# Performance work log

Measured on AMD Instinct MI355X. Metric: run time of the kernel, lower is better.

The kernel has to match this reference:

```python
import jax, jax.numpy as jnp
import numpy as np

B, H, W, CIN, COUT, KH, KW = 16, 64, 64, 256, 256, 3, 3


def setup_inputs() -> dict:
    key = jax.random.key(0)
    k1, k2, k3 = jax.random.split(key, 3)
    x = jax.random.normal(k1, (B, H, W, CIN), dtype=jnp.float32)
    style = jax.random.normal(k2, (B, CIN), dtype=jnp.float32)
    # glorot-ish scale for the base kernel
    kernel = jax.random.normal(k3, (KH, KW, CIN, COUT), dtype=jnp.float32) * 0.05
    return {"x": x, "style": style, "kernel": kernel}


def reference(x, style, kernel):
    b = x.shape[0]
    cout = kernel.shape[-1]
    # Modulate: per-sample weights [B, kh, kw, Cin, Cout]
    w = kernel[None] * (style[:, None, None, :, None] + 1.0)
    # Demodulate: L2 normalize over (kh, kw, Cin) per (sample, out-channel)
    w = w / jnp.sqrt(jnp.sum(jnp.square(w), axis=(1, 2, 3), keepdims=True) + 1e-8)
    # Batch-as-groups grouped conv: x -> [1, B*Cin, H, W]
    xg = jnp.transpose(x, (0, 3, 1, 2)).reshape(1, -1, x.shape[1], x.shape[2])
    # w -> [kh, kw, Cin, B*Cout]
    wg = jnp.transpose(w, (1, 2, 3, 0, 4)).reshape(w.shape[1], w.shape[2], w.shape[3], -1)
    y = jax.lax.conv_general_dilated(
        xg, wg,
        window_strides=(1, 1),
        padding='SAME',
        dimension_numbers=('NCHW', 'HWIO', 'NCHW'),
        feature_group_count=b,
    )
    # [1, B*Cout, H, W] -> [B, H, W, Cout]
    y = y.reshape(b, cout, y.shape[2], y.shape[3])
    return jnp.transpose(y, (0, 2, 3, 1))
```

## Files before the change

### kernel.cpp

```cpp
#include <hip/hip_runtime.h>


#define HH 64
#define WW 64
#define CI 256
#define CO 256
#define KTOT 2304
#define CIPITCH 40
#define XCOLS 66
#define BPITCH 100

typedef float    f32x4 __attribute__((ext_vector_type(4)));
typedef _Float16 f16x8 __attribute__((ext_vector_type(8)));
typedef __fp16   fp16x2 __attribute__((ext_vector_type(2)));

__device__ __forceinline__ unsigned pk2(float a, float b) {
    fp16x2 h = __builtin_amdgcn_cvt_pkrtz(a, b);
    return __builtin_bit_cast(unsigned, h);
}

__global__ __launch_bounds__(256) void modscale_part(
    const float* __restrict__ kern,
    const float* __restrict__ style,
    float* __restrict__ scale2)
{
    const int b = blockIdx.x / 9;
    const int t = blockIdx.x - b * 9;
    const int tid = threadIdx.x;
    __shared__ float st[CI];
    st[tid] = style[b * CI + tid] + 1.0f;
    __syncthreads();
    float acc = 0.f;
    const float* kp = kern + (size_t)t * CI * CO + tid;
    #pragma unroll 8
    for (int ci = 0; ci < CI; ++ci) {
        float m = kp[ci * CO] * st[ci];
        acc += m * m;
    }
    atomicAdd(&scale2[b * CO + tid], acc);
}

__global__ __launch_bounds__(256) void prep_wt(const float* __restrict__ kern,
                                               ushort* __restrict__ Wt) {
    __shared__ ushort tile[64][65];
    const int kt = blockIdx.x >> 2;
    const int ct = blockIdx.x & 3;
    const int k0 = kt * 64, c0 = ct * 64;
    const int tid = threadIdx.x;
    const int r = tid >> 2, q = tid & 3;

    const float* src = kern + (size_t)(k0 + r) * CO + c0 + q * 16;
    #pragma unroll
    for (int j = 0; j < 16; ++j) {
        _Float16 h = (_Float16)src[j];
        tile[q * 16 + j][r] = __builtin_bit_cast(unsigned short, h);
    }
    __syncthreads();
    ushort* dst = Wt + (size_t)(c0 + r) * KTOT + k0 + q * 16;
    #pragma unroll
    for (int j = 0; j < 16; ++j) dst[j] = tile[r][q * 16 + j];
}

__global__ __launch_bounds__(256) void gemm_conv(
    const float* __restrict__ x,
    const ushort* __restrict__ Wt,
    const float* __restrict__ style,
    const float* __restrict__ scale2,
    float* __restrict__ y)
{
    __shared__ __align__(16) ushort xs[4 * XCOLS * CIPITCH];
    __shared__ __align__(16) ushort bs[128 * BPITCH];
    __shared__ float s_style[CI];

    const int tid  = threadIdx.x;
    const int lane = tid & 63;
    const int wave = tid >> 6;

    const int mtile = blockIdx.x >> 1;
    const int n0    = (blockIdx.x & 1) * 128;
    const int p0    = mtile * 128;
    const int b     = p0 >> 12;
    const int h0    = (p0 >> 6) & 63;

    s_style[tid] = style[b * CI + tid] + 1.0f;

    const int wm = (wave & 1) * 64;
    const int wn = (wave >> 1) * 64;
    const int fr = lane & 15;
    const int fq = lane >> 4;
    const int xlane = fr * CIPITCH + fq * 8;

    f32x4 acc[4][4] = {};

    for (int c = 0; c < 8; ++c) {
        __syncthreads();

        #pragma unroll
        for (int p = 0; p < 9; ++p) {
            const int task = p * 256 + tid;
            if (task < 2112) {
                const int rowcol = task >> 3;
                const int chunk  = task & 7;
                const int row = rowcol / XCOLS;
                const int col = rowcol - row * XCOLS;
                const int rg = h0 - 1 + row;
                const int cg = col - 1;
                f32x4 v = {0.f, 0.f, 0.f, 0.f};
                if ((unsigned)rg < 64u && (unsigned)cg < 64u)
                    v = *(const f32x4*)(x + ((size_t)((b * HH + rg) * WW + cg)) * CI
                                          + c * 32 + chunk * 4);
                const f32x4 st = *(const f32x4*)(s_style + c * 32 + chunk * 4);
                const f32x4 m = v * st;
                uint2 u;
                u.x = pk2(m.x, m.y);
                u.y = pk2(m.z, m.w);
                *(uint2*)(xs + rowcol * CIPITCH + chunk * 4) = u;
            }
        }

        #pragma unroll
        for (int tr = 0; tr < 3; ++tr) {
            if (tr) __syncthreads();

            #pragma unroll
            for (int p = 0; p < 6; ++p) {
                const int task = p * 256 + tid;
                const int co = task / 12;
                const int r  = task - co * 12;
                const int tl = r >> 2;
                const int ch = r & 3;
                const uint4 v = *(const uint4*)(Wt + (size_t)(n0 + co) * KTOT
                                                + (tr * 3 + tl) * 256 + c * 32 + ch * 8);
                *(uint4*)(bs + co * BPITCH + tl * 32 + ch * 8) = v;
            }
            __syncthreads();

            #pragma unroll
            for (int tl = 0; tl < 3; ++tl) {
                const int t  = tr * 3 + tl;
                const int dh = t / 3;
                const int dw = t - dh * 3;

                f16x8 af[4], bf[4];
                #pragma unroll
                for (int i = 0; i < 4; ++i) {
                    const int mb   = wm + i * 16;
                    const int mrow = (mb >> 6) + dh;
                    const int mcol = (mb & 63) + dw;
                    af[i] = *(const f16x8*)(xs + (mrow * XCOLS + mcol) * CIPITCH + xlane);
                }
                #pragma unroll
                for (int j = 0; j < 4; ++j)
                    bf[j] = *(const f16x8*)(bs + (wn + j * 16 + fr) * BPITCH
                                            + tl * 32 + fq * 8);
                #pragma unroll
                for (int i = 0; i < 4; ++i)
                    #pragma unroll
                    for (int j = 0; j < 4; ++j)
                        acc[i][j] = __builtin_amdgcn_mfma_f32_16x16x32_f16(
                            af[i], bf[j], acc[i][j], 0, 0, 0);
            }
        }
    }

    float sc[4];
    #pragma unroll
    for (int j = 0; j < 4; ++j)
        sc[j] = __frsqrt_rn(scale2[b * CO + n0 + wn + j * 16 + fr] + 1e-8f);
    #pragma unroll
    for (int i = 0; i < 4; ++i) {
        const int m_base = p0 + wm + i * 16 + fq * 4;
        #pragma unroll
        for (int j = 0; j < 4; ++j) {
            float* yp = y + (size_t)m_base * CO + n0 + wn + j * 16 + fr;
            #pragma unroll
            for (int r = 0; r < 4; ++r)
                yp[(size_t)r * CO] = acc[i][j][r] * sc[j];
        }
    }
}

extern "C" void kernel_launch(void* const* d_in, const int* in_sizes, int n_in,
                              void* d_out, int out_size, void* d_ws, size_t ws_size,
                              hipStream_t stream) {
    const float* x     = (const float*)d_in[0];
    const float* style = (const float*)d_in[1];
    const float* kern  = (const float*)d_in[2];
    float* out = (float*)d_out;

    float*  scale2 = (float*)d_ws;
    ushort* Wt     = (ushort*)((char*)d_ws + 16384);

    hipMemsetAsync(scale2, 0, 16 * CO * sizeof(float), stream);
    modscale_part<<<16 * 9, 256, 0, stream>>>(kern, style, scale2);
    prep_wt<<<144, 256, 0, stream>>>(kern, Wt);
    gemm_conv<<<512 * 2, 256, 0, stream>>>(x, Wt, style, scale2, out);
}
```

Measured before the change: 243.7 us.

## Double-buffer activation tiles, read weights directly from global, fuse demod scale

The GEMM conv kernel now double-buffers the modulated fp16 activation tile in shared memory, staging the next channel chunk while computing the current one. It drops the shared-memory weight tile and its per-tap-row barriers, loading B fragments straight from global and relying on L2/L1 caching. The modulation-norm kernel is rebuilt as one 1024-thread block per sample with a shared-memory reduction, and it emits the final rsqrt directly, which removes the memset and the atomics. The trade-off is that weight loads now hit global memory without coalescing across the tile, and shared memory use doubles for activations.

```diff
diff --git a/kernel.cpp b/kernel.cpp
--- a/kernel.cpp
+++ b/kernel.cpp
@@ -8,7 +8,7 @@
 #define KTOT 2304
 #define CIPITCH 40
 #define XCOLS 66
-#define BPITCH 100
+#define XSSZ (4 * XCOLS * CIPITCH)
 
 typedef float    f32x4 __attribute__((ext_vector_type(4)));
 typedef _Float16 f16x8 __attribute__((ext_vector_type(8)));
@@ -19,25 +19,37 @@
     return __builtin_bit_cast(unsigned, h);
 }
 
-__global__ __launch_bounds__(256) void modscale_part(
+__global__ __launch_bounds__(1024) void modscale_kernel(
     const float* __restrict__ kern,
     const float* __restrict__ style,
-    float* __restrict__ scale2)
+    float* __restrict__ scale)
 {
-    const int b = blockIdx.x / 9;
-    const int t = blockIdx.x - b * 9;
+    const int b   = blockIdx.x;
     const int tid = threadIdx.x;
-    __shared__ float st[CI];
-    st[tid] = style[b * CI + tid] + 1.0f;
+    const int co  = tid & 255;
+    const int q   = tid >> 8;
+
+    __shared__ float s_style[CI];
+    __shared__ float s_part[1024];
+
+    if (tid < CI) s_style[tid] = style[b * CI + tid] + 1.0f;
     __syncthreads();
+
     float acc = 0.f;
-    const float* kp = kern + (size_t)t * CI * CO + tid;
-    #pragma unroll 8
-    for (int ci = 0; ci < CI; ++ci) {
-        float m = kp[ci * CO] * st[ci];
-        acc += m * m;
+    for (int t = 0; t < 9; ++t) {
+        const float* kp = kern + (size_t)t * CI * CO + co;
+        #pragma unroll 4
+        for (int ci = q * 64; ci < q * 64 + 64; ++ci) {
+            float m = kp[ci * CO] * s_style[ci];
+            acc += m * m;
+        }
     }
-    atomicAdd(&scale2[b * CO + tid], acc);
+    s_part[tid] = acc;
+    __syncthreads();
+    if (q == 0) {
+        float s = s_part[co] + s_part[256 + co] + s_part[512 + co] + s_part[768 + co];
+        scale[b * CO + co] = 1.0f / sqrtf(s + 1e-8f);
+    }
 }
 
 __global__ __launch_bounds__(256) void prep_wt(const float* __restrict__ kern,
@@ -65,11 +77,10 @@
     const float* __restrict__ x,
     const ushort* __restrict__ Wt,
     const float* __restrict__ style,
-    const float* __restrict__ scale2,
+    const float* __restrict__ scale,
     float* __restrict__ y)
 {
-    __shared__ __align__(16) ushort xs[4 * XCOLS * CIPITCH];
-    __shared__ __align__(16) ushort bs[128 * BPITCH];
+    __shared__ __align__(16) ushort xs[2 * XSSZ];
     __shared__ float s_style[CI];
 
     const int tid  = threadIdx.x;
@@ -88,13 +99,12 @@
     const int wn = (wave >> 1) * 64;
     const int fr = lane & 15;
     const int fq = lane >> 4;
+    const int wrow  = wm >> 6;
     const int xlane = fr * CIPITCH + fq * 8;
+    const ushort* wbase = Wt + (size_t)(n0 + wn + fr) * KTOT + fq * 8;
 
-    f32x4 acc[4][4] = {};
-
-    for (int c = 0; c < 8; ++c) {
-        __syncthreads();
-
+    auto stage = [&](int c, int buf) {
+        ushort* dst = xs + buf * XSSZ;
         #pragma unroll
         for (int p = 0; p < 9; ++p) {
             const int task = p * 256 + tid;
@@ -114,59 +124,48 @@
                 uint2 u;
                 u.x = pk2(m.x, m.y);
                 u.y = pk2(m.z, m.w);
-                *(uint2*)(xs + rowcol * CIPITCH + chunk * 4) = u;
+                *(uint2*)(dst + rowcol * CIPITCH + chunk * 4) = u;
             }
         }
+    };
+
+    f32x4 acc[4][4] = {};
+
+    __syncthreads();
+    stage(0, 0);
+
+    for (int c = 0; c < 8; ++c) {
+        __syncthreads();
+        if (c < 7) stage(c + 1, (c + 1) & 1);
+
+        const ushort* xb = xs + (c & 1) * XSSZ;
+        const ushort* wb = wbase + c * 32;
 
         #pragma unroll
-        for (int tr = 0; tr < 3; ++tr) {
-            if (tr) __syncthreads();
-
+        for (int t = 0; t < 9; ++t) {
+            const int dh = t / 3;
+            const int dw = t - dh * 3;
+            f16x8 af[4], bf[4];
+            const ushort* ab = xb + ((wrow + dh) * XCOLS + dw) * CIPITCH + xlane;
             #pragma unroll
-            for (int p = 0; p < 6; ++p) {
-                const int task = p * 256 + tid;
-                const int co = task / 12;
-                const int r  = task - co * 12;
-                const int tl = r >> 2;
-                const int ch = r & 3;
-                const uint4 v = *(const uint4*)(Wt + (size_t)(n0 + co) * KTOT
-                                                + (tr * 3 + tl) * 256 + c * 32 + ch * 8);
-                *(uint4*)(bs + co * BPITCH + tl * 32 + ch * 8) = v;
-            }
-            __syncthreads();
-
+            for (int i = 0; i < 4; ++i)
+                af[i] = *(const f16x8*)(ab + i * 16 * CIPITCH);
             #pragma unroll
-            for (int tl = 0; tl < 3; ++tl) {
-                const int t  = tr * 3 + tl;
-                const int dh = t / 3;
-                const int dw = t - dh * 3;
-
-                f16x8 af[4], bf[4];
-                #pragma unroll
-                for (int i = 0; i < 4; ++i) {
-                    const int mb   = wm + i * 16;
-                    const int mrow = (mb >> 6) + dh;
-                    const int mcol = (mb & 63) + dw;
-                    af[i] = *(const f16x8*)(xs + (mrow * XCOLS + mcol) * CIPITCH + xlane);
-                }
+            for (int j = 0; j < 4; ++j)
+                bf[j] = *(const f16x8*)(wb + (size_t)j * 16 * KTOT + t * 256);
+            #pragma unroll
+            for (int i = 0; i < 4; ++i)
                 #pragma unroll
                 for (int j = 0; j < 4; ++j)
-                    bf[j] = *(const f16x8*)(bs + (wn + j * 16 + fr) * BPITCH
-                                            + tl * 32 + fq * 8);
-                #pragma unroll
-                for (int i = 0; i < 4; ++i)
-                    #pragma unroll
-                    for (int j = 0; j < 4; ++j)
-                        acc[i][j] = __builtin_amdgcn_mfma_f32_16x16x32_f16(
-                            af[i], bf[j], acc[i][j], 0, 0, 0);
-            }
+                    acc[i][j] = __builtin_amdgcn_mfma_f32_16x16x32_f16(
+                        af[i], bf[j], acc[i][j], 0, 0, 0);
         }
     }
 
     float sc[4];
     #pragma unroll
     for (int j = 0; j < 4; ++j)
-        sc[j] = __frsqrt_rn(scale2[b * CO + n0 + wn + j * 16 + fr] + 1e-8f);
+        sc[j] = scale[b * CO + n0 + wn + j * 16 + fr];
     #pragma unroll
     for (int i = 0; i < 4; ++i) {
         const int m_base = p0 + wm + i * 16 + fq * 4;
@@ -188,11 +187,10 @@
     const float* kern  = (const float*)d_in[2];
     float* out = (float*)d_out;
 
-    float*  scale2 = (float*)d_ws;
-    ushort* Wt     = (ushort*)((char*)d_ws + 16384);
+    float*  scale = (float*)d_ws;
+    ushort* Wt    = (ushort*)((char*)d_ws + 16384);
 
-    hipMemsetAsync(scale2, 0, 16 * CO * sizeof(float), stream);
-    modscale_part<<<16 * 9, 256, 0, stream>>>(kern, style, scale2);
+    modscale_kernel<<<16, 1024, 0, stream>>>(kern, style, scale);
     prep_wt<<<144, 256, 0, stream>>>(kern, Wt);
-    gemm_conv<<<512 * 2, 256, 0, stream>>>(x, Wt, style, scale2, out);
+    gemm_conv<<<512 * 2, 256, 0, stream>>>(x, Wt, style, scale, out);
 }
```

Result: slower. 333.1 us (+36.7%).

## Double-buffer LDS staging, widen tile to full Cout, relayout weights per tap

Applied to the files above, without the earlier changes.

Each block now covers all 256 output channels, so the grid shrinks to 512 blocks and every staged activation tile is reused for twice as many MFMAs. Weights are stored in a [cin-slice][tap][cout][32] layout so each tap's B tile is one contiguous 16 KB load. Both A and B LDS buffers are double-buffered, and the next slice is prefetched while MFMAs run, with one barrier per tap. The trade-offs are a doubled accumulator count per wave (128 regs) with launch_bounds(256,2), a larger LDS footprint, and fewer blocks in flight to hide latency.

```diff
diff --git a/kernel.cpp b/kernel.cpp
--- a/kernel.cpp
+++ b/kernel.cpp
@@ -5,10 +5,10 @@
 #define WW 64
 #define CI 256
 #define CO 256
-#define KTOT 2304
-#define CIPITCH 40
+#define PITCH 36
 #define XCOLS 66
-#define BPITCH 100
+#define XSSZ (4 * XCOLS * PITCH)
+#define BSSZ (256 * PITCH)
 
 typedef float    f32x4 __attribute__((ext_vector_type(4)));
 typedef _Float16 f16x8 __attribute__((ext_vector_type(8)));
@@ -41,7 +41,7 @@
 }
 
 __global__ __launch_bounds__(256) void prep_wt(const float* __restrict__ kern,
-                                               ushort* __restrict__ Wt) {
+                                               ushort* __restrict__ Wt2) {
     __shared__ ushort tile[64][65];
     const int kt = blockIdx.x >> 2;
     const int ct = blockIdx.x & 3;
@@ -56,51 +56,52 @@
         tile[q * 16 + j][r] = __builtin_bit_cast(unsigned short, h);
     }
     __syncthreads();
-    ushort* dst = Wt + (size_t)(c0 + r) * KTOT + k0 + q * 16;
+    const int kbase = k0 + q * 16;
+    const int t  = kbase >> 8;
+    const int ci = kbase & 255;
+    const int cs = ci >> 5;
+    const int kk = ci & 31;
+    ushort* dst = Wt2 + (((size_t)(cs * 9 + t) * 256 + c0 + r) * 32 + kk);
     #pragma unroll
     for (int j = 0; j < 16; ++j) dst[j] = tile[r][q * 16 + j];
 }
 
-__global__ __launch_bounds__(256) void gemm_conv(
+__global__ __launch_bounds__(256, 2) void gemm_conv(
     const float* __restrict__ x,
-    const ushort* __restrict__ Wt,
+    const ushort* __restrict__ Wt2,
     const float* __restrict__ style,
     const float* __restrict__ scale2,
     float* __restrict__ y)
 {
-    __shared__ __align__(16) ushort xs[4 * XCOLS * CIPITCH];
-    __shared__ __align__(16) ushort bs[128 * BPITCH];
+    __shared__ __align__(16) ushort xs[2 * XSSZ];
+    __shared__ __align__(16) ushort bs[2 * BSSZ];
     __shared__ float s_style[CI];
 
     const int tid  = threadIdx.x;
     const int lane = tid & 63;
     const int wave = tid >> 6;
 
-    const int mtile = blockIdx.x >> 1;
-    const int n0    = (blockIdx.x & 1) * 128;
-    const int p0    = mtile * 128;
-    const int b     = p0 >> 12;
-    const int h0    = (p0 >> 6) & 63;
+    const int p0 = blockIdx.x * 128;
+    const int b  = p0 >> 12;
+    const int h0 = (p0 >> 6) & 63;
 
     s_style[tid] = style[b * CI + tid] + 1.0f;
 
     const int wm = (wave & 1) * 64;
-    const int wn = (wave >> 1) * 64;
+    const int wn = (wave >> 1) * 128;
     const int fr = lane & 15;
     const int fq = lane >> 4;
-    const int xlane = fr * CIPITCH + fq * 8;
-
-    f32x4 acc[4][4] = {};
-
-    for (int c = 0; c < 8; ++c) {
-        __syncthreads();
-
+    const int wrow  = wm >> 6;
+    const int xlane = fq * 8;
+
+    auto stage_xs_chunk = [&](int c, int buf, int chunk3) {
+        ushort* dst = xs + buf * XSSZ;
         #pragma unroll
-        for (int p = 0; p < 9; ++p) {
+        for (int p = chunk3 * 3; p < chunk3 * 3 + 3; ++p) {
             const int task = p * 256 + tid;
             if (task < 2112) {
                 const int rowcol = task >> 3;
-                const int chunk  = task & 7;
+                const int ch  = task & 7;
                 const int row = rowcol / XCOLS;
                 const int col = rowcol - row * XCOLS;
                 const int rg = h0 - 1 + row;
@@ -108,71 +109,80 @@
                 f32x4 v = {0.f, 0.f, 0.f, 0.f};
                 if ((unsigned)rg < 64u && (unsigned)cg < 64u)
                     v = *(const f32x4*)(x + ((size_t)((b * HH + rg) * WW + cg)) * CI
-                                          + c * 32 + chunk * 4);
-                const f32x4 st = *(const f32x4*)(s_style + c * 32 + chunk * 4);
+                                          + c * 32 + ch * 4);
+                const f32x4 st = *(const f32x4*)(s_style + c * 32 + ch * 4);
                 const f32x4 m = v * st;
                 uint2 u;
                 u.x = pk2(m.x, m.y);
                 u.y = pk2(m.z, m.w);
-                *(uint2*)(xs + rowcol * CIPITCH + chunk * 4) = u;
+                *(uint2*)(dst + rowcol * PITCH + ch * 4) = u;
             }
         }
-
+    };
+
+    auto stage_bs = [&](int l, int buf) {
+        const ushort* src = Wt2 + (size_t)l * 8192 + tid * 32;
+        uint4 v0 = *(const uint4*)(src);
+        uint4 v1 = *(const uint4*)(src + 8);
+        uint4 v2 = *(const uint4*)(src + 16);
+        uint4 v3 = *(const uint4*)(src + 24);
+        ushort* dst = bs + buf * BSSZ + tid * PITCH;
+        *(uint4*)(dst)      = v0;
+        *(uint4*)(dst + 8)  = v1;
+        *(uint4*)(dst + 16) = v2;
+        *(uint4*)(dst + 24) = v3;
+    };
+
+    f32x4 acc[4][8] = {};
+
+    __syncthreads();
+
+    stage_xs_chunk(0, 0, 0);
+    stage_xs_chunk(0, 0, 1);
+    stage_xs_chunk(0, 0, 2);
+    stage_bs(0, 0);
+    __syncthreads();
+
+    for (int c = 0; c < 8; ++c) {
+        const ushort* xb = xs + (c & 1) * XSSZ;
         #pragma unroll
-        for (int tr = 0; tr < 3; ++tr) {
-            if (tr) __syncthreads();
-
-            #pragma unroll
-            for (int p = 0; p < 6; ++p) {
-                const int task = p * 256 + tid;
-                const int co = task / 12;
-                const int r  = task - co * 12;
-                const int tl = r >> 2;
-                const int ch = r & 3;
-                const uint4 v = *(const uint4*)(Wt + (size_t)(n0 + co) * KTOT
-                                                + (tr * 3 + tl) * 256 + c * 32 + ch * 8);
-                *(uint4*)(bs + co * BPITCH + tl * 32 + ch * 8) = v;
-            }
+        for (int t = 0; t < 9; ++t) {
+            const int l = c * 9 + t;
+            if (l < 71) stage_bs(l + 1, (l + 1) & 1);
+            if (c < 7 && t < 3) stage_xs_chunk(c + 1, (c + 1) & 1, t);
+
+            const ushort* bsb = bs + (l & 1) * BSSZ;
+            const int dh = t / 3;
+            const int dw = t - dh * 3;
+
+            f16x8 af[4], bf[8];
+            const ushort* ab = xb + ((wrow + dh) * XCOLS + fr + dw) * PITCH + xlane;
+            #pragma unroll
+            for (int i = 0; i < 4; ++i)
+                af[i] = *(const f16x8*)(ab + i * 16 * PITCH);
+            #pragma unroll
+            for (int j = 0; j < 8; ++j)
+                bf[j] = *(const f16x8*)(bsb + (wn + j * 16 + fr) * PITCH + fq * 8);
+            #pragma unroll
+            for (int i = 0; i < 4; ++i)
+                #pragma unroll
+                for (int j = 0; j < 8; ++j)
+                    acc[i][j] = __builtin_amdgcn_mfma_f32_16x16x32_f16(
+                        af[i], bf[j], acc[i][j], 0, 0, 0);
             __syncthreads();
-
-            #pragma unroll
-            for (int tl = 0; tl < 3; ++tl) {
-                const int t  = tr * 3 + tl;
-                const int dh = t / 3;
-                const int dw = t - dh * 3;
-
-                f16x8 af[4], bf[4];
-                #pragma unroll
-                for (int i = 0; i < 4; ++i) {
-                    const int mb   = wm + i * 16;
-                    const int mrow = (mb >> 6) + dh;
-                    const int mcol = (mb & 63) + dw;
-                    af[i] = *(const f16x8*)(xs + (mrow * XCOLS + mcol) * CIPITCH + xlane);
-                }
-                #pragma unroll
-                for (int j = 0; j < 4; ++j)
-                    bf[j] = *(const f16x8*)(bs + (wn + j * 16 + fr) * BPITCH
-                                            + tl * 32 + fq * 8);
-                #pragma unroll
-                for (int i = 0; i < 4; ++i)
-                    #pragma unroll
-                    for (int j = 0; j < 4; ++j)
-                        acc[i][j] = __builtin_amdgcn_mfma_f32_16x16x32_f16(
-                            af[i], bf[j], acc[i][j], 0, 0, 0);
-            }
         }
     }
 
-    float sc[4];
-    #pragma unroll
-    for (int j = 0; j < 4; ++j)
-        sc[j] = __frsqrt_rn(scale2[b * CO + n0 + wn + j * 16 + fr] + 1e-8f);
+    float sc[8];
+    #pragma unroll
+    for (int j = 0; j < 8; ++j)
+        sc[j] = __frsqrt_rn(scale2[b * CO + wn + j * 16 + fr] + 1e-8f);
     #pragma unroll
     for (int i = 0; i < 4; ++i) {
         const int m_base = p0 + wm + i * 16 + fq * 4;
         #pragma unroll
-        for (int j = 0; j < 4; ++j) {
-            float* yp = y + (size_t)m_base * CO + n0 + wn + j * 16 + fr;
+        for (int j = 0; j < 8; ++j) {
+            float* yp = y + (size_t)m_base * CO + wn + j * 16 + fr;
             #pragma unroll
             for (int r = 0; r < 4; ++r)
                 yp[(size_t)r * CO] = acc[i][j][r] * sc[j];
@@ -189,10 +199,10 @@
     float* out = (float*)d_out;
 
     float*  scale2 = (float*)d_ws;
-    ushort* Wt     = (ushort*)((char*)d_ws + 16384);
+    ushort* Wt2    = (ushort*)((char*)d_ws + 16384);
 
     hipMemsetAsync(scale2, 0, 16 * CO * sizeof(float), stream);
     modscale_part<<<16 * 9, 256, 0, stream>>>(kern, style, scale2);
-    prep_wt<<<144, 256, 0, stream>>>(kern, Wt);
-    gemm_conv<<<512 * 2, 256, 0, stream>>>(x, Wt, style, scale2, out);
-}
+    prep_wt<<<144, 256, 0, stream>>>(kern, Wt2);
+    gemm_conv<<<512, 256, 0, stream>>>(x, Wt2, style, scale2, out);
+}
```

Result: slower. 409.8 us (+68.1%).
